# Kernel optimization log

Measured on AMD Instinct MI355X. Metric: run time of the kernel, lower is better.

Reference implementation:

```python
import jax, jax.numpy as jnp
import numpy as np

C = 512
GROUPS = 32
EPS = 1e-6


def setup_inputs() -> dict:
    key = jax.random.key(0)
    ks = jax.random.split(key, 10)
    B, H, W = 4, 64, 64
    s = 1.0 / np.sqrt(C)
    return {
        "x": jax.random.normal(ks[0], (B, C, H, W), dtype=jnp.float32),
        "gn_weight": jnp.ones((C,), jnp.float32),
        "gn_bias": jnp.zeros((C,), jnp.float32),
        "Wq": jax.random.normal(ks[1], (C, C), jnp.float32) * s,
        "bq": jnp.zeros((C,), jnp.float32),
        "Wk": jax.random.normal(ks[2], (C, C), jnp.float32) * s,
        "bk": jnp.zeros((C,), jnp.float32),
        "Wv": jax.random.normal(ks[3], (C, C), jnp.float32) * s,
        "bv": jnp.zeros((C,), jnp.float32),
        "Wo": jax.random.normal(ks[4], (C, C), jnp.float32) * s,
        "bo": jnp.zeros((C,), jnp.float32),
    }


def _group_norm(x, weight, bias):
    B, Ch, H, W = x.shape
    xg = x.reshape(B, GROUPS, Ch // GROUPS, H, W)
    mean = jnp.mean(xg, axis=(2, 3, 4), keepdims=True)
    var = jnp.var(xg, axis=(2, 3, 4), keepdims=True)
    xg = (xg - mean) * jax.lax.rsqrt(var + EPS)
    h = xg.reshape(B, Ch, H, W)
    return h * weight[None, :, None, None] + bias[None, :, None, None]


def reference(x, gn_weight, gn_bias, Wq, bq, Wk, bk, Wv, bv, Wo, bo):
    B, Ch, H, W = x.shape
    h = _group_norm(x, gn_weight, gn_bias)
    # [B, N, C] with N = H*W spatial tokens
    h = h.reshape(B, Ch, H * W).transpose(0, 2, 1)
    q = h @ Wq.T + bq
    k = h @ Wk.T + bk
    v = h @ Wv.T + bv
    scale = 1.0 / jnp.sqrt(jnp.asarray(Ch, x.dtype))
    scores = jnp.einsum("bnc,bmc->bnm", q, k) * scale  # [B, N, N]
    attn = jax.nn.softmax(scores, axis=-1)
    out = jnp.einsum("bnm,bmc->bnc", attn, v)
    out = out @ Wo.T + bo  # Dropout(0.0) is identity
    out = out.transpose(0, 2, 1).reshape(B, Ch, H, W)
    return x + out
```

## Files before the change

### kernel.cpp

```cpp
#include <hip/hip_runtime.h>
#include <hip/hip_bf16.h>

typedef __attribute__((ext_vector_type(8))) short bf16x8;
typedef __attribute__((ext_vector_type(4))) short bf16x4;
typedef __attribute__((ext_vector_type(4))) float f32x4;

__device__ __forceinline__ short f2bf(float f){
  __hip_bfloat16 h = __float2bfloat16(f);
  return __builtin_bit_cast(short, h);
}
__device__ __forceinline__ float bf2f(short s){
  unsigned u = ((unsigned)(unsigned short)s) << 16;
  return __builtin_bit_cast(float, u);
}

__device__ __forceinline__ void gload_lds16(const short* g, char* l){
  __builtin_amdgcn_global_load_lds(
      (const __attribute__((address_space(1))) void*)g,
      (__attribute__((address_space(3))) void*)l, 16, 0, 0);
}

#define SB0() __builtin_amdgcn_sched_barrier(0)
#define BARRIER() do{ SB0(); __builtin_amdgcn_s_barrier(); }while(0)

__global__ __launch_bounds__(256) void gn_stats(const float* __restrict__ x,
                                                float* __restrict__ stats){
  int b = blockIdx.x >> 5, g = blockIdx.x & 31;
  const float4* p = (const float4*)(x + ((long long)b*512 + g*16)*4096);
  float s = 0.f, s2 = 0.f;
  for (int i = threadIdx.x; i < 16384; i += 256){
    float4 v = p[i];
    s  += v.x + v.y + v.z + v.w;
    s2 += v.x*v.x + v.y*v.y + v.z*v.z + v.w*v.w;
  }
  #pragma unroll
  for (int o = 32; o; o >>= 1){ s += __shfl_xor(s, o); s2 += __shfl_xor(s2, o); }
  __shared__ float rs[4], rs2[4];
  int wid = threadIdx.x >> 6;
  if ((threadIdx.x & 63) == 0){ rs[wid] = s; rs2[wid] = s2; }
  __syncthreads();
  if (threadIdx.x == 0){
    float S  = rs[0]+rs[1]+rs[2]+rs[3];
    float S2 = rs2[0]+rs2[1]+rs2[2]+rs2[3];
    float mean = S * (1.f/65536.f);
    float var  = S2 * (1.f/65536.f) - mean*mean;
    stats[blockIdx.x*2]   = mean;
    stats[blockIdx.x*2+1] = rsqrtf(var + 1e-6f);
  }
}

__global__ __launch_bounds__(256) void gn_apply(const float* __restrict__ x,
                                                const float* __restrict__ stats,
                                                const float* __restrict__ gw,
                                                const float* __restrict__ gb,
                                                short* __restrict__ h){
  __shared__ float tile[128][65];
  int b  = blockIdx.y;
  int n0 = blockIdx.x * 64;
  int t  = threadIdx.x;
  const float* xb = x + (long long)b*512*4096;
  for (int cc = 0; cc < 4; cc++){
    int c0 = cc*128;
    #pragma unroll
    for (int r = 0; r < 128; r += 4){
      int c = r + (t >> 6);
      tile[c][t & 63] = xb[(long long)(c0+c)*4096 + n0 + (t & 63)];
    }
    __syncthreads();
    int n = t >> 2, cp = (t & 3)*32;
    short tmp[32];
    #pragma unroll
    for (int j = 0; j < 32; j++){
      int c = c0 + cp + j;
      float mean = stats[(b*32 + (c >> 4))*2];
      float rstd = stats[(b*32 + (c >> 4))*2 + 1];
      float v = (tile[cp+j][n] - mean)*rstd*gw[c] + gb[c];
      tmp[j] = f2bf(v);
    }
    long long ho = ((long long)b*4096 + n0 + n)*512 + c0 + cp;
    #pragma unroll
    for (int j2 = 0; j2 < 4; j2++){
      bf16x8 v8;
      #pragma unroll
      for (int e = 0; e < 8; e++) v8[e] = tmp[j2*8 + e];
      *(bf16x8*)&h[ho + j2*8] = v8;
    }
    __syncthreads();
  }
}

__global__ __launch_bounds__(256) void f2bf_all(
    const float* __restrict__ w0, const float* __restrict__ w1,
    const float* __restrict__ w2, const float* __restrict__ w3,
    short* __restrict__ o0, short* __restrict__ o1,
    short* __restrict__ o2, short* __restrict__ o3){
  int idx = blockIdx.x*256 + threadIdx.x;
  int m = idx >> 15, r = idx & 32767;
  const float* src = (m==0) ? w0 : (m==1) ? w1 : (m==2) ? w2 : w3;
  short* dst       = (m==0) ? o0 : (m==1) ? o1 : (m==2) ? o2 : o3;
  const float4* p = (const float4*)src + (long long)r*2;
  float4 a = p[0], c = p[1];
  bf16x8 v;
  v[0]=f2bf(a.x); v[1]=f2bf(a.y); v[2]=f2bf(a.z); v[3]=f2bf(a.w);
  v[4]=f2bf(c.x); v[5]=f2bf(c.y); v[6]=f2bf(c.z); v[7]=f2bf(c.w);
  *(bf16x8*)&dst[(long long)r*8] = v;
}

__global__ __launch_bounds__(256) void softmax_rows(short* __restrict__ S){
  long long row = blockIdx.x;
  short* p = S + row*4096;
  int t = threadIdx.x;
  bf16x8 v0 = *(bf16x8*)&p[t*16];
  bf16x8 v1 = *(bf16x8*)&p[t*16 + 8];
  float f[16];
  #pragma unroll
  for (int e = 0; e < 8; e++){ f[e] = bf2f(v0[e]); f[8+e] = bf2f(v1[e]); }
  float m = f[0];
  #pragma unroll
  for (int e = 1; e < 16; e++) m = fmaxf(m, f[e]);
  #pragma unroll
  for (int o = 32; o; o >>= 1) m = fmaxf(m, __shfl_xor(m, o));
  __shared__ float red[4];
  int wid = t >> 6;
  if ((t & 63) == 0) red[wid] = m;
  __syncthreads();
  m = fmaxf(fmaxf(red[0], red[1]), fmaxf(red[2], red[3]));
  float s = 0.f;
  #pragma unroll
  for (int e = 0; e < 16; e++){ f[e] = exp2f((f[e]-m)*1.4426950408889634f); s += f[e]; }
  #pragma unroll
  for (int o = 32; o; o >>= 1) s += __shfl_xor(s, o);
  __syncthreads();
  if ((t & 63) == 0) red[wid] = s;
  __syncthreads();
  s = red[0]+red[1]+red[2]+red[3];
  float inv = 1.f/s;
  #pragma unroll
  for (int e = 0; e < 8; e++){ v0[e] = f2bf(f[e]*inv); v1[e] = f2bf(f[8+e]*inv); }
  *(bf16x8*)&p[t*16]     = v0;
  *(bf16x8*)&p[t*16 + 8] = v1;
}

template<int MODE, int BN, bool SWZ>
__global__ __launch_bounds__(512, 2) void gemmF(
    const short* __restrict__ A, const short* __restrict__ Bw,
    const float* __restrict__ bias,
    void* __restrict__ outp, const float* __restrict__ resid,
    int M, int Nn, int Kd,
    long long sA, long long sB, long long sO, float scale)
{
  constexpr int WARPS_N = BN/64;
  constexpr int WARPS_M = 8/WARPS_N;
  constexpr int WM = 256/WARPS_M;
  constexpr int MF = WM/16;
  constexpr int QR = MF/4;
  constexpr int ABYT = 32768;
  constexpr int BBYT = BN*128;
  constexpr int BUFSZ = ABYT + BBYT;
  constexpr int BH = BBYT/16384;
  extern __shared__ char smem[];

  int bx, by, bz;
  if constexpr (SWZ){
    int id = blockIdx.x;
    int xcd = id & 7, s = id >> 3;
    int bxh = s >> 6, rem = s & 63;
    bx = xcd*2 + bxh; by = rem & 15; bz = rem >> 4;
  } else { bx = blockIdx.x; by = blockIdx.y; bz = blockIdx.z; }

  const short* Ab = A + bz*sA;
  const short* Bb = Bw + bz*sB;
  const int m0 = bx*256, n0 = by*BN;
  const int t = threadIdx.x;
  const int lane = t & 63, wid = t >> 6;
  const int g = lane >> 4, lr = lane & 15;
  const int wr = wid / WARPS_N, wc = wid % WARPS_N;
  const long long KdLL = Kd;

  const int r0 = t >> 3, c8 = t & 7;

  auto STAGE_A = [&](int kt, int buf, int h){
    char* d = smem + buf*BUFSZ + h*16384 + t*16;
    #pragma unroll
    for (int j = 0; j < 2; j++){
      int row = h*128 + j*64 + r0;
      gload_lds16(Ab + (long long)(m0+row)*KdLL + (long long)kt*64 + ((c8 ^ (row&7))*8),
                  d + j*8192);
    }
  };
  auto STAGE_B = [&](int kt, int buf, int h){
    char* d = smem + buf*BUFSZ + ABYT + h*16384 + t*16;
    #pragma unroll
    for (int j = 0; j < 2; j++){
      int row = h*128 + j*64 + r0;
      gload_lds16(Bb + (long long)(n0+row)*KdLL + (long long)kt*64 + ((c8 ^ (row&7))*8),
                  d + j*8192);
    }
  };

  int roA[MF], swA[MF], roB[4], swB[4];
  #pragma unroll
  for (int mf = 0; mf < MF; mf++){
    int ra = wr*WM + mf*16 + lr;
    roA[mf] = (ra>>7)*16384 + (ra&127)*128; swA[mf] = ra & 7;
  }
  #pragma unroll
  for (int nf = 0; nf < 4; nf++){
    int rb = wc*64 + nf*16 + lr;
    roB[nf] = ABYT + (rb>>7)*16384 + (rb&127)*128; swB[nf] = rb & 7;
  }

  f32x4 acc[MF][4];
  #pragma unroll
  for (int i = 0; i < MF; i++)
    #pragma unroll
    for (int j = 0; j < 4; j++)
      acc[i][j] = f32x4{0.f,0.f,0.f,0.f};
  bf16x8 av[2][QR][2], bv[4][2];

  #define RD_AV(SET, Q, BASE) do{                                         \
    _Pragma("unroll")                                                     \
    for (int _i = 0; _i < QR; _i++)                                       \
      _Pragma("unroll")                                                   \
      for (int _ks = 0; _ks < 2; _ks++){                                  \
        int _x = (Q)*QR + _i;                                             \
        av[SET][_i][_ks] = *(const bf16x8*)((BASE) + roA[_x] +            \
                            (((_ks*4+g) ^ swA[_x])<<4));                  \
      } }while(0)

  #define RD_BV(BASE) do{                                                 \
    _Pragma("unroll")                                                     \
    for (int _n = 0; _n < 4; _n++)                                        \
      _Pragma("unroll")                                                   \
      for (int _ks = 0; _ks < 2; _ks++)                                   \
        bv[_n][_ks] = *(const bf16x8*)((BASE) + roB[_n] +                 \
                            (((_ks*4+g) ^ swB[_n])<<4));                  \
    }while(0)

  #define MFMA_PH(Q, SET) do{                                             \
    __builtin_amdgcn_s_setprio(1);                                        \
    _Pragma("unroll")                                                     \
    for (int _ks = 0; _ks < 2; _ks++)                                     \
      _Pragma("unroll")                                                   \
      for (int _n = 0; _n < 4; _n++)                                      \
        _Pragma("unroll")                                                 \
        for (int _i = 0; _i < QR; _i++){                                  \
          if constexpr (MODE == 0)                                        \
            acc[(Q)*QR+_i][_n] = __builtin_amdgcn_mfma_f32_16x16x32_bf16( \
              bv[_n][_ks], av[SET][_i][_ks], acc[(Q)*QR+_i][_n], 0,0,0);  \
          else                                                            \
            acc[(Q)*QR+_i][_n] = __builtin_amdgcn_mfma_f32_16x16x32_bf16( \
              av[SET][_i][_ks], bv[_n][_ks], acc[(Q)*QR+_i][_n], 0,0,0);  \
        }                                                                 \
    __builtin_amdgcn_s_setprio(0); }while(0)

  #define WAIT_LGKM_JI() do{                                              \
    if constexpr (QR == 2) asm volatile("s_waitcnt lgkmcnt(4)":::"memory");\
    else                   asm volatile("s_waitcnt lgkmcnt(2)":::"memory");\
    SB0(); }while(0)

  const int NT = Kd >> 6;

  STAGE_A(0,0,0); STAGE_A(0,0,1);
  STAGE_B(0,0,0); if constexpr (BH==2) STAGE_B(0,0,1);
  STAGE_B(1,1,0); if constexpr (BH==2) STAGE_B(1,1,1);
  if constexpr (BH==2) asm volatile("s_waitcnt vmcnt(4)":::"memory");
  else                 asm volatile("s_waitcnt vmcnt(2)":::"memory");
  SB0();
  __builtin_amdgcn_s_barrier();
  RD_AV(0, 0, smem);

  for (int kt = 0; kt < NT; ++kt){
    char* bc  = smem + (kt & 1)*BUFSZ;
    char* bn_ = smem + ((kt & 1)^1)*BUFSZ;
    RD_BV(bc);
    RD_AV(1, 1, bc);
    if (kt+1 < NT) STAGE_A(kt+1, (kt&1)^1, 0);
    BARRIER();
    WAIT_LGKM_JI();
    MFMA_PH(0, 0);
    BARRIER();
    RD_AV(0, 2, bc);
    if (kt+1 < NT) STAGE_A(kt+1, (kt&1)^1, 1);
    BARRIER();
    WAIT_LGKM_JI();
    MFMA_PH(1, 1);
    BARRIER();
    RD_AV(1, 3, bc);
    if (kt+2 < NT) STAGE_B(kt+2, kt&1, 0);
    BARRIER();
    if (kt+2 < NT) asm volatile("s_waitcnt vmcnt(2)":::"memory");
    else           asm volatile("s_waitcnt vmcnt(0)":::"memory");
    SB0();
    WAIT_LGKM_JI();
    MFMA_PH(2, 0);
    BARRIER();
    if (kt+1 < NT) RD_AV(0, 0, bn_);
    if constexpr (BH==2){ if (kt+2 < NT) STAGE_B(kt+2, kt&1, 1); }
    BARRIER();
    if (kt+1 < NT){ WAIT_LGKM_JI(); }
    else { asm volatile("s_waitcnt lgkmcnt(0)":::"memory"); SB0(); }
    MFMA_PH(3, 1);
    BARRIER();
  }

  if constexpr (MODE == 0){
    short* outb = (short*)outp + bz*sO;
    const bool hb = (bias != nullptr);
    #pragma unroll
    for (int mi = 0; mi < MF; mi++){
      int row = m0 + wr*WM + mi*16 + lr;
      #pragma unroll
      for (int ni = 0; ni < 4; ni++){
        int col = n0 + wc*64 + ni*16 + g*4;
        float b0=0.f,b1=0.f,b2=0.f,b3=0.f;
        if (hb){ float4 bb = *(const float4*)&bias[col]; b0=bb.x; b1=bb.y; b2=bb.z; b3=bb.w; }
        bf16x4 pk;
        pk[0] = f2bf((acc[mi][ni][0] + b0)*scale);
        pk[1] = f2bf((acc[mi][ni][1] + b1)*scale);
        pk[2] = f2bf((acc[mi][ni][2] + b2)*scale);
        pk[3] = f2bf((acc[mi][ni][3] + b3)*scale);
        *(bf16x4*)&outb[(long long)row*Nn + col] = pk;
      }
    }
  } else if constexpr (MODE == 1){
    short* outb = (short*)outp + bz*sO;
    #pragma unroll
    for (int ni = 0; ni < 4; ni++){
      int col = n0 + wc*64 + ni*16 + lr;
      float bv2 = bias ? bias[col] : 0.f;
      #pragma unroll
      for (int mi = 0; mi < MF; mi++){
        int row = m0 + wr*WM + mi*16 + g*4;
        bf16x4 pk;
        #pragma unroll
        for (int i = 0; i < 4; i++) pk[i] = f2bf((acc[mi][ni][i] + bv2)*scale);
        *(bf16x4*)&outb[(long long)col*M + row] = pk;
      }
    }
  } else {
    float* outb = (float*)outp + bz*sO;
    const float* rx = resid + bz*sO;
    #pragma unroll
    for (int ni = 0; ni < 4; ni++){
      int col = n0 + wc*64 + ni*16 + lr;
      float bv2 = bias[col];
      #pragma unroll
      for (int mi = 0; mi < MF; mi++){
        int row = m0 + wr*WM + mi*16 + g*4;
        long long off = (long long)col*M + row;
        float4 xr = *(const float4*)&rx[off];
        float4 o;
        o.x = acc[mi][ni][0] + bv2 + xr.x;
        o.y = acc[mi][ni][1] + bv2 + xr.y;
        o.z = acc[mi][ni][2] + bv2 + xr.z;
        o.w = acc[mi][ni][3] + bv2 + xr.w;
        *(float4*)&outb[off] = o;
      }
    }
  }
  #undef RD_AV
  #undef RD_BV
  #undef MFMA_PH
  #undef WAIT_LGKM_JI
}

extern "C" void kernel_launch(void* const* d_in, const int* in_sizes, int n_in,
                              void* d_out, int out_size, void* d_ws, size_t ws_size,
                              hipStream_t stream)
{
  const float* x   = (const float*)d_in[0];
  const float* gnw = (const float*)d_in[1];
  const float* gnb = (const float*)d_in[2];
  const float* Wq  = (const float*)d_in[3];
  const float* bq  = (const float*)d_in[4];
  const float* Wk  = (const float*)d_in[5];
  const float* bk  = (const float*)d_in[6];
  const float* Wv  = (const float*)d_in[7];
  const float* bvp = (const float*)d_in[8];
  const float* Wo  = (const float*)d_in[9];
  const float* bo  = (const float*)d_in[10];
  float* out = (float*)d_out;

  char* ws = (char*)d_ws;
  const size_t MB = 1ull << 20;
  short* h    = (short*)(ws);
  short* q    = (short*)(ws + 16*MB);
  short* kmat = (short*)(ws + 32*MB);
  short* vt   = (short*)(ws + 48*MB);
  short* ao   = (short*)(ws + 64*MB);
  short* wqb  = (short*)(ws + 80*MB);
  short* wkb  = wqb + 262144;
  short* wvb  = wkb + 262144;
  short* wob  = wvb + 262144;
  float* stats= (float*)(ws + 82*MB);
  short* S    = (short*)(ws + 84*MB);

  const int LDS256 = 131072, LDS128 = 98304;
  hipFuncSetAttribute(reinterpret_cast<const void*>(&gemmF<0,256,true>),
                      hipFuncAttributeMaxDynamicSharedMemorySize, LDS256);
  hipFuncSetAttribute(reinterpret_cast<const void*>(&gemmF<0,256,false>),
                      hipFuncAttributeMaxDynamicSharedMemorySize, LDS256);
  hipFuncSetAttribute(reinterpret_cast<const void*>(&gemmF<0,128,false>),
                      hipFuncAttributeMaxDynamicSharedMemorySize, LDS128);
  hipFuncSetAttribute(reinterpret_cast<const void*>(&gemmF<1,128,false>),
                      hipFuncAttributeMaxDynamicSharedMemorySize, LDS128);
  hipFuncSetAttribute(reinterpret_cast<const void*>(&gemmF<2,128,false>),
                      hipFuncAttributeMaxDynamicSharedMemorySize, LDS128);

  dim3 blk(256);
  dim3 blk512(512);
  gn_stats<<<dim3(128), blk, 0, stream>>>(x, stats);
  gn_apply<<<dim3(64,4), blk, 0, stream>>>(x, stats, gnw, gnb, h);
  f2bf_all<<<dim3(512), blk, 0, stream>>>(Wq, Wk, Wv, Wo, wqb, wkb, wvb, wob);

  const long long sTok = 4096ll*512;
  const long long sS   = 4096ll*4096;
  const float qscale = 0.044194173824159216f;

  gemmF<0,128,false><<<dim3(16,4,4), blk512, LDS128, stream>>>(h, wqb, bq,  q,    nullptr, 4096, 512, 512, sTok, 0, sTok, qscale);
  gemmF<0,128,false><<<dim3(16,4,4), blk512, LDS128, stream>>>(h, wkb, bk,  kmat, nullptr, 4096, 512, 512, sTok, 0, sTok, 1.f);
  gemmF<1,128,false><<<dim3(16,4,4), blk512, LDS128, stream>>>(h, wvb, bvp, vt,   nullptr, 4096, 512, 512, sTok, 0, sTok, 1.f);

  if (ws_size >= 212*MB){
    gemmF<0,256,true><<<dim3(1024), blk512, LDS256, stream>>>(q, kmat, nullptr, S, nullptr, 4096, 4096, 512, sTok, sTok, sS, 1.f);
    softmax_rows<<<dim3(16384), blk, 0, stream>>>(S);
    gemmF<0,128,false><<<dim3(16,4,4), blk512, LDS128, stream>>>(S, vt, nullptr, ao, nullptr, 4096, 512, 4096, sS, sTok, sTok, 1.f);
  } else {
    for (int b = 0; b < 4; b++){
      gemmF<0,256,false><<<dim3(16,16,1), blk512, LDS256, stream>>>(q + b*sTok, kmat + b*sTok, nullptr, S, nullptr, 4096, 4096, 512, 0, 0, 0, 1.f);
      softmax_rows<<<dim3(4096), blk, 0, stream>>>(S);
      gemmF<0,128,false><<<dim3(16,4,1), blk512, LDS128, stream>>>(S, vt + b*sTok, nullptr, ao + b*sTok, nullptr, 4096, 512, 4096, 0, 0, 0, 1.f);
    }
  }

  gemmF<2,128,false><<<dim3(16,4,4), blk512, LDS128, stream>>>(ao, wob, bo, out, x, 4096, 512, 512, sTok, 0, sTok, 1.f);
}
```

Before: 360.7 us.

## Fuse softmax exp into QK GEMM epilogue and defer normalization to PV GEMM

Removes the standalone softmax pass over the score matrix. The QK GEMM epilogue now writes exp(scores) and per-tile partial row sums, a small kernel reduces those sums into inverse denominators, and the PV GEMM epilogue scales each output row by its inverse. This is meant to avoid a full read and write of the large bf16 score matrix. The exponent is taken without subtracting the row max, so it could overflow if scores grow large. New block swizzles are also added for the QK and PV launches to group tiles per XCD.

```diff
diff --git a/kernel.cpp b/kernel.cpp
--- a/kernel.cpp
+++ b/kernel.cpp
@@ -106,48 +106,25 @@
   *(bf16x8*)&dst[(long long)r*8] = v;
 }
 
-__global__ __launch_bounds__(256) void softmax_rows(short* __restrict__ S){
-  long long row = blockIdx.x;
-  short* p = S + row*4096;
-  int t = threadIdx.x;
-  bf16x8 v0 = *(bf16x8*)&p[t*16];
-  bf16x8 v1 = *(bf16x8*)&p[t*16 + 8];
-  float f[16];
-  #pragma unroll
-  for (int e = 0; e < 8; e++){ f[e] = bf2f(v0[e]); f[8+e] = bf2f(v1[e]); }
-  float m = f[0];
-  #pragma unroll
-  for (int e = 1; e < 16; e++) m = fmaxf(m, f[e]);
-  #pragma unroll
-  for (int o = 32; o; o >>= 1) m = fmaxf(m, __shfl_xor(m, o));
-  __shared__ float red[4];
-  int wid = t >> 6;
-  if ((t & 63) == 0) red[wid] = m;
-  __syncthreads();
-  m = fmaxf(fmaxf(red[0], red[1]), fmaxf(red[2], red[3]));
-  float s = 0.f;
-  #pragma unroll
-  for (int e = 0; e < 16; e++){ f[e] = exp2f((f[e]-m)*1.4426950408889634f); s += f[e]; }
-  #pragma unroll
-  for (int o = 32; o; o >>= 1) s += __shfl_xor(s, o);
-  __syncthreads();
-  if ((t & 63) == 0) red[wid] = s;
-  __syncthreads();
-  s = red[0]+red[1]+red[2]+red[3];
-  float inv = 1.f/s;
-  #pragma unroll
-  for (int e = 0; e < 8; e++){ v0[e] = f2bf(f[e]*inv); v1[e] = f2bf(f[8+e]*inv); }
-  *(bf16x8*)&p[t*16]     = v0;
-  *(bf16x8*)&p[t*16 + 8] = v1;
-}
-
-template<int MODE, int BN, bool SWZ>
+__global__ __launch_bounds__(256) void reduce_den(const float* __restrict__ partial,
+                                                  float* __restrict__ inv_den,
+                                                  int nrows){
+  int r = blockIdx.x*256 + threadIdx.x;
+  if (r >= nrows) return;
+  const float4* p = (const float4*)(partial + (long long)r*16);
+  float4 a = p[0], b = p[1], c = p[2], d = p[3];
+  float s = a.x+a.y+a.z+a.w + b.x+b.y+b.z+b.w + c.x+c.y+c.z+c.w + d.x+d.y+d.z+d.w;
+  inv_den[r] = 1.f / s;
+}
+
+template<int MODE, int BN, int SWZ>
 __global__ __launch_bounds__(512, 2) void gemmF(
     const short* __restrict__ A, const short* __restrict__ Bw,
     const float* __restrict__ bias,
     void* __restrict__ outp, const float* __restrict__ resid,
     int M, int Nn, int Kd,
-    long long sA, long long sB, long long sO, float scale)
+    long long sA, long long sB, long long sO, float scale,
+    const float* __restrict__ dptr, float* __restrict__ partial)
 {
   constexpr int WARPS_N = BN/64;
   constexpr int WARPS_M = 8/WARPS_N;
@@ -161,11 +138,20 @@
   extern __shared__ char smem[];
 
   int bx, by, bz;
-  if constexpr (SWZ){
+  if constexpr (SWZ == 1){
     int id = blockIdx.x;
     int xcd = id & 7, s = id >> 3;
-    int bxh = s >> 6, rem = s & 63;
-    bx = xcd*2 + bxh; by = rem & 15; bz = rem >> 4;
+    int region = xcd + ((s >> 4) << 3);
+    int o = s & 15;
+    bz = region >> 4;
+    bx = (region & 3)*4 + (o & 3);
+    by = ((region >> 2) & 3)*4 + (o >> 2);
+  } else if constexpr (SWZ == 2){
+    int id = blockIdx.x;
+    int xcd = id & 7, s = id >> 3;
+    int combo = xcd*2 + (s & 1);
+    by = combo & 3; bz = combo >> 2;
+    bx = s >> 1;
   } else { bx = blockIdx.x; by = blockIdx.y; bz = blockIdx.z; }
 
   const short* Ab = A + bz*sA;
@@ -245,12 +231,12 @@
       for (int _n = 0; _n < 4; _n++)                                      \
         _Pragma("unroll")                                                 \
         for (int _i = 0; _i < QR; _i++){                                  \
-          if constexpr (MODE == 0)                                        \
+          if constexpr (MODE == 1 || MODE == 2)                           \
+            acc[(Q)*QR+_i][_n] = __builtin_amdgcn_mfma_f32_16x16x32_bf16( \
+              av[SET][_i][_ks], bv[_n][_ks], acc[(Q)*QR+_i][_n], 0,0,0);  \
+          else                                                            \
             acc[(Q)*QR+_i][_n] = __builtin_amdgcn_mfma_f32_16x16x32_bf16( \
               bv[_n][_ks], av[SET][_i][_ks], acc[(Q)*QR+_i][_n], 0,0,0);  \
-          else                                                            \
-            acc[(Q)*QR+_i][_n] = __builtin_amdgcn_mfma_f32_16x16x32_bf16( \
-              av[SET][_i][_ks], bv[_n][_ks], acc[(Q)*QR+_i][_n], 0,0,0);  \
         }                                                                 \
     __builtin_amdgcn_s_setprio(0); }while(0)
 
@@ -320,6 +306,54 @@
         pk[1] = f2bf((acc[mi][ni][1] + b1)*scale);
         pk[2] = f2bf((acc[mi][ni][2] + b2)*scale);
         pk[3] = f2bf((acc[mi][ni][3] + b3)*scale);
+        *(bf16x4*)&outb[(long long)row*Nn + col] = pk;
+      }
+    }
+  } else if constexpr (MODE == 4){
+    short* outb = (short*)outp + bz*sO;
+    float* rowpart = (float*)smem;
+    constexpr float LOG2E = 1.4426950408889634f;
+    #pragma unroll
+    for (int mi = 0; mi < MF; mi++){
+      int lrow = wr*WM + mi*16 + lr;
+      int row  = m0 + lrow;
+      float rs = 0.f;
+      #pragma unroll
+      for (int ni = 0; ni < 4; ni++){
+        int col = n0 + wc*64 + ni*16 + g*4;
+        bf16x4 pk;
+        #pragma unroll
+        for (int i = 0; i < 4; i++){
+          float p = exp2f(acc[mi][ni][i]*LOG2E);
+          rs += p;
+          pk[i] = f2bf(p);
+        }
+        *(bf16x4*)&outb[(long long)row*Nn + col] = pk;
+      }
+      rs += __shfl_xor(rs, 16);
+      rs += __shfl_xor(rs, 32);
+      if (g == 0) rowpart[lrow*WARPS_N + wc] = rs;
+    }
+    __syncthreads();
+    if (t < 256){
+      float s2 = 0.f;
+      #pragma unroll
+      for (int j = 0; j < WARPS_N; j++) s2 += rowpart[t*WARPS_N + j];
+      partial[((long long)bz*4096 + m0 + t)*16 + by] = s2;
+    }
+  } else if constexpr (MODE == 5){
+    short* outb = (short*)outp + bz*sO;
+    const float* dd = dptr + (long long)bz*M;
+    #pragma unroll
+    for (int mi = 0; mi < MF; mi++){
+      int row = m0 + wr*WM + mi*16 + lr;
+      float inv = dd[row];
+      #pragma unroll
+      for (int ni = 0; ni < 4; ni++){
+        int col = n0 + wc*64 + ni*16 + g*4;
+        bf16x4 pk;
+        #pragma unroll
+        for (int i = 0; i < 4; i++) pk[i] = f2bf(acc[mi][ni][i]*inv);
         *(bf16x4*)&outb[(long long)row*Nn + col] = pk;
       }
     }
@@ -384,28 +418,34 @@
 
   char* ws = (char*)d_ws;
   const size_t MB = 1ull << 20;
-  short* h    = (short*)(ws);
-  short* q    = (short*)(ws + 16*MB);
-  short* kmat = (short*)(ws + 32*MB);
-  short* vt   = (short*)(ws + 48*MB);
-  short* ao   = (short*)(ws + 64*MB);
-  short* wqb  = (short*)(ws + 80*MB);
-  short* wkb  = wqb + 262144;
-  short* wvb  = wkb + 262144;
-  short* wob  = wvb + 262144;
-  float* stats= (float*)(ws + 82*MB);
-  short* S    = (short*)(ws + 84*MB);
+  short* h      = (short*)(ws);
+  short* q      = (short*)(ws + 16*MB);
+  short* kmat   = (short*)(ws + 32*MB);
+  short* vt     = (short*)(ws + 48*MB);
+  short* ao     = (short*)(ws + 64*MB);
+  short* wqb    = (short*)(ws + 80*MB);
+  short* wkb    = wqb + 262144;
+  short* wvb    = wkb + 262144;
+  short* wob    = wvb + 262144;
+  float* stats  = (float*)(ws + 82*MB);
+  float* inv_den= (float*)(ws + 82*MB + 8192);
+  float* partial= (float*)(ws + 83*MB);
+  short* S      = (short*)(ws + 84*MB);
 
   const int LDS256 = 131072, LDS128 = 98304;
-  hipFuncSetAttribute(reinterpret_cast<const void*>(&gemmF<0,256,true>),
+  hipFuncSetAttribute(reinterpret_cast<const void*>(&gemmF<4,256,1>),
                       hipFuncAttributeMaxDynamicSharedMemorySize, LDS256);
-  hipFuncSetAttribute(reinterpret_cast<const void*>(&gemmF<0,256,false>),
+  hipFuncSetAttribute(reinterpret_cast<const void*>(&gemmF<4,256,0>),
                       hipFuncAttributeMaxDynamicSharedMemorySize, LDS256);
-  hipFuncSetAttribute(reinterpret_cast<const void*>(&gemmF<0,128,false>),
+  hipFuncSetAttribute(reinterpret_cast<const void*>(&gemmF<0,128,0>),
                       hipFuncAttributeMaxDynamicSharedMemorySize, LDS128);
-  hipFuncSetAttribute(reinterpret_cast<const void*>(&gemmF<1,128,false>),
+  hipFuncSetAttribute(reinterpret_cast<const void*>(&gemmF<1,128,0>),
                       hipFuncAttributeMaxDynamicSharedMemorySize, LDS128);
-  hipFuncSetAttribute(reinterpret_cast<const void*>(&gemmF<2,128,false>),
+  hipFuncSetAttribute(reinterpret_cast<const void*>(&gemmF<2,128,0>),
+                      hipFuncAttributeMaxDynamicSharedMemorySize, LDS128);
+  hipFuncSetAttribute(reinterpret_cast<const void*>(&gemmF<5,128,2>),
+                      hipFuncAttributeMaxDynamicSharedMemorySize, LDS128);
+  hipFuncSetAttribute(reinterpret_cast<const void*>(&gemmF<5,128,0>),
                       hipFuncAttributeMaxDynamicSharedMemorySize, LDS128);
 
   dim3 blk(256);
@@ -418,21 +458,21 @@
   const long long sS   = 4096ll*4096;
   const float qscale = 0.044194173824159216f;
 
-  gemmF<0,128,false><<<dim3(16,4,4), blk512, LDS128, stream>>>(h, wqb, bq,  q,    nullptr, 4096, 512, 512, sTok, 0, sTok, qscale);
-  gemmF<0,128,false><<<dim3(16,4,4), blk512, LDS128, stream>>>(h, wkb, bk,  kmat, nullptr, 4096, 512, 512, sTok, 0, sTok, 1.f);
-  gemmF<1,128,false><<<dim3(16,4,4), blk512, LDS128, stream>>>(h, wvb, bvp, vt,   nullptr, 4096, 512, 512, sTok, 0, sTok, 1.f);
+  gemmF<0,128,0><<<dim3(16,4,4), blk512, LDS128, stream>>>(h, wqb, bq,  q,    nullptr, 4096, 512, 512, sTok, 0, sTok, qscale, nullptr, nullptr);
+  gemmF<0,128,0><<<dim3(16,4,4), blk512, LDS128, stream>>>(h, wkb, bk,  kmat, nullptr, 4096, 512, 512, sTok, 0, sTok, 1.f, nullptr, nullptr);
+  gemmF<1,128,0><<<dim3(16,4,4), blk512, LDS128, stream>>>(h, wvb, bvp, vt,   nullptr, 4096, 512, 512, sTok, 0, sTok, 1.f, nullptr, nullptr);
 
   if (ws_size >= 212*MB){
-    gemmF<0,256,true><<<dim3(1024), blk512, LDS256, stream>>>(q, kmat, nullptr, S, nullptr, 4096, 4096, 512, sTok, sTok, sS, 1.f);
-    softmax_rows<<<dim3(16384), blk, 0, stream>>>(S);
-    gemmF<0,128,false><<<dim3(16,4,4), blk512, LDS128, stream>>>(S, vt, nullptr, ao, nullptr, 4096, 512, 4096, sS, sTok, sTok, 1.f);
+    gemmF<4,256,1><<<dim3(1024), blk512, LDS256, stream>>>(q, kmat, nullptr, S, nullptr, 4096, 4096, 512, sTok, sTok, sS, 1.f, nullptr, partial);
+    reduce_den<<<dim3(64), blk, 0, stream>>>(partial, inv_den, 16384);
+    gemmF<5,128,2><<<dim3(256), blk512, LDS128, stream>>>(S, vt, nullptr, ao, nullptr, 4096, 512, 4096, sS, sTok, sTok, 1.f, inv_den, nullptr);
   } else {
     for (int b = 0; b < 4; b++){
-      gemmF<0,256,false><<<dim3(16,16,1), blk512, LDS256, stream>>>(q + b*sTok, kmat + b*sTok, nullptr, S, nullptr, 4096, 4096, 512, 0, 0, 0, 1.f);
-      softmax_rows<<<dim3(4096), blk, 0, stream>>>(S);
-      gemmF<0,128,false><<<dim3(16,4,1), blk512, LDS128, stream>>>(S, vt + b*sTok, nullptr, ao + b*sTok, nullptr, 4096, 512, 4096, 0, 0, 0, 1.f);
-    }
-  }
-
-  gemmF<2,128,false><<<dim3(16,4,4), blk512, LDS128, stream>>>(ao, wob, bo, out, x, 4096, 512, 512, sTok, 0, sTok, 1.f);
-}
+      gemmF<4,256,0><<<dim3(16,16,1), blk512, LDS256, stream>>>(q + b*sTok, kmat + b*sTok, nullptr, S, nullptr, 4096, 4096, 512, 0, 0, 0, 1.f, nullptr, partial);
+      reduce_den<<<dim3(16), blk, 0, stream>>>(partial, inv_den, 4096);
+      gemmF<5,128,0><<<dim3(16,4,1), blk512, LDS128, stream>>>(S, vt + b*sTok, nullptr, ao + b*sTok, nullptr, 4096, 512, 4096, 0, 0, 0, 1.f, inv_den, nullptr);
+    }
+  }
+
+  gemmF<2,128,0><<<dim3(16,4,4), blk512, LDS128, stream>>>(ao, wob, bo, out, x, 4096, 512, 512, sTok, 0, sTok, 1.f, nullptr, nullptr);
+}
```

Result: faster. 318.1 us (-11.8%).
